# Kernel optimization log

Measured on AMD Instinct MI355X. Metric: run time of the kernel, lower is better.

## Reference

```python
import jax, jax.numpy as jnp
import numpy as np

B, TT, TS, H, O = 16, 512, 512, 1024, 1024


def setup_inputs() -> dict:
    key = jax.random.key(0)
    k1, k2, k3, k4, k5 = jax.random.split(key, 5)
    ht = jax.random.normal(k1, (B, TT, H), dtype=jnp.float32)
    hs = jax.random.normal(k2, (B, TS, H), dtype=jnp.float32)
    source = jax.random.randint(k3, (B, TS), 0, 10000, dtype=jnp.int32)
    # glorot-like scaling for weights
    W_a = jax.random.normal(k4, (H, H), dtype=jnp.float32) * (2.0 / (H + H)) ** 0.5
    W_c = jax.random.normal(k5, (2 * H, O), dtype=jnp.float32) * (2.0 / (2 * H + O)) ** 0.5
    b = jnp.zeros((O,), dtype=jnp.float32)
    return {"ht": ht, "hs": hs, "source": source, "W_a": W_a, "W_c": W_c, "b": b}


def reference(ht, hs, source, W_a, W_c, b):
    # score = ht . (hs @ W_a)^T : [B, Tt, Ts]
    keys = jnp.einsum('bsk,kl->bsl', hs, W_a)
    score = jnp.einsum('btk,bsk->bts', ht, keys)
    # stable exp with max subtraction (matches original manual softmax)
    score = jnp.exp(score - jnp.max(score, axis=-1, keepdims=True))
    # sequence mask from count of non-pad (non-zero) source tokens
    lens = jnp.sum((source != 0).astype(jnp.int32), axis=1)          # [B]
    mask = (jnp.arange(TS)[None, :] < lens[:, None]).astype(score.dtype)  # [B, Ts]
    score = score * mask[:, None, :]
    a = score / jnp.sum(score, axis=-1, keepdims=True)               # [B, Tt, Ts]
    c = jnp.einsum('bts,bsk->btk', a, hs)                            # context [B, Tt, H]
    h = jnp.concatenate([c, ht], axis=-1)                            # [B, Tt, 2H]
    return jnp.tanh(jnp.einsum('btk,kl->btl', h, W_c) + b)
```

## Files before the change

### kernel.cpp

```cpp
#include <hip/hip_runtime.h>
#include <math.h>

typedef unsigned short u16;
typedef unsigned int u32;

using f32x4 = __attribute__((ext_vector_type(4))) float;
using s16x8 = __attribute__((ext_vector_type(8))) short;
using f16x8 = __attribute__((ext_vector_type(8))) _Float16;
using u32x4 = __attribute__((ext_vector_type(4))) u32;

#define DEVI static __device__ __forceinline__

#define BB 16
#define TT 512
#define TS 512
#define HH 1024
#define OO 1024

DEVI void split_bf(float x, u16& hb, u16& lb) {
    u32 xb = __float_as_uint(x);
    float hf = __uint_as_float(xb & 0xffff0000u);
    hb = (u16)(xb >> 16);
    lb = (u16)(__float_as_uint(x - hf) >> 16);
}

DEVI float ub(u16 h) { return __uint_as_float((u32)h << 16); }

template <int PREC> struct FragT;
template <> struct FragT<0> { using T = s16x8; };
template <> struct FragT<1> { using T = f16x8; };

DEVI f32x4 mfma16(s16x8 a, s16x8 b, f32x4 c) {
    return __builtin_amdgcn_mfma_f32_16x16x32_bf16(a, b, c, 0, 0, 0);
}
DEVI f32x4 mfma16(f16x8 a, f16x8 b, f32x4 c) {
    return __builtin_amdgcn_mfma_f32_16x16x32_f16(a, b, c, 0, 0, 0);
}

DEVI void gl16(const void* g, void* l) {
    __builtin_amdgcn_global_load_lds(
        (__attribute__((address_space(1))) const void*)g,
        (__attribute__((address_space(3))) void*)l, 16, 0, 0);
}

__global__ void prep1_kernel(const float* __restrict__ hs,
                             u16* __restrict__ rhi, u16* __restrict__ rlo,
                             u16* __restrict__ thi,
                             const float* __restrict__ Wa,
                             u16* __restrict__ whi, u16* __restrict__ wlo,
                             const int* __restrict__ src, int* __restrict__ lens) {
    __shared__ float tile[32][33];
    __shared__ int part[4];
    int id = blockIdx.x;
    int tid = threadIdx.x;
    int tx = tid & 31, ty = tid >> 5;
    if (id < 8192) {
        int bx = id & 31, by = (id >> 5) & 15, bz = id >> 9;
        long boff = (long)bz * TS * HH;
        const float* s = hs + boff;
        u16* rh = rhi + boff;
        u16* rl = rlo + boff;
        u16* th = thi + boff;
        int c0 = bx * 32, r0 = by * 32;
#pragma unroll
        for (int i = 0; i < 32; i += 8) {
            long o = (long)(r0 + ty + i) * HH + (c0 + tx);
            float v = s[o];
            tile[ty + i][tx] = v;
            u16 hb, lb;
            split_bf(v, hb, lb);
            rh[o] = hb;
            rl[o] = lb;
        }
        __syncthreads();
#pragma unroll
        for (int i = 0; i < 32; i += 8) {
            long o = (long)(c0 + ty + i) * TS + (r0 + tx);
            th[o] = __builtin_bit_cast(u16, (_Float16)tile[tx][ty + i]);
        }
    } else if (id < 8192 + 1024) {
        int id2 = id - 8192;
        int bx = id2 & 31, by = id2 >> 5;
        int c0 = bx * 32, r0 = by * 32;
#pragma unroll
        for (int i = 0; i < 32; i += 8)
            tile[ty + i][tx] = Wa[(long)(r0 + ty + i) * HH + (c0 + tx)];
        __syncthreads();
#pragma unroll
        for (int i = 0; i < 32; i += 8) {
            u16 hb, lb;
            split_bf(tile[tx][ty + i], hb, lb);
            long o = (long)(c0 + ty + i) * HH + (r0 + tx);
            whi[o] = hb;
            wlo[o] = lb;
        }
    } else {
        int b = id - (8192 + 1024);
        int v0 = (src[b * TS + tid] != 0) ? 1 : 0;
        int v1 = (src[b * TS + 256 + tid] != 0) ? 1 : 0;
        unsigned long long m0 = __ballot(v0);
        unsigned long long m1 = __ballot(v1);
        if ((tid & 63) == 0) part[tid >> 6] = __popcll(m0) + __popcll(m1);
        __syncthreads();
        if (tid == 0) lens[b] = part[0] + part[1] + part[2] + part[3];
    }
}

__global__ void prep2_kernel(const float* __restrict__ ht, u16* __restrict__ htF,
                             const float* __restrict__ Wc, u16* __restrict__ wcthi) {
    __shared__ float tile[32][33];
    int id = blockIdx.x;
    int tid = threadIdx.x;
    if (id < 4096) {
        long i = ((long)id * 256 + tid) * 8;
        float4 v0 = *(const float4*)(ht + i);
        float4 v1 = *(const float4*)(ht + i + 4);
        float fv[8] = {v0.x, v0.y, v0.z, v0.w, v1.x, v1.y, v1.z, v1.w};
        f16x8 o;
#pragma unroll
        for (int j = 0; j < 8; ++j) o[j] = (_Float16)fv[j];
        *(f16x8*)(htF + i) = o;
    } else {
        int id2 = id - 4096;
        int bx = id2 & 31, by = id2 >> 5;
        int tx = tid & 31, ty = tid >> 5;
        int c0 = bx * 32, r0 = by * 32;
#pragma unroll
        for (int i = 0; i < 32; i += 8)
            tile[ty + i][tx] = Wc[(long)(r0 + ty + i) * OO + (c0 + tx)];
        __syncthreads();
#pragma unroll
        for (int i = 0; i < 32; i += 8) {
            long o = (long)(c0 + ty + i) * (2 * HH) + (r0 + tx);
            wcthi[o] = __builtin_bit_cast(u16, (_Float16)tile[tx][ty + i]);
        }
    }
}

__global__ void softmax_mask_kernel(u16* __restrict__ h0, u16* __restrict__ l0,
                                    const u16* __restrict__ h1, const u16* __restrict__ l1,
                                    const int* __restrict__ lens) {
    long row = blockIdx.x;
    int len = lens[blockIdx.x >> 9];
    int lane = threadIdx.x;
    long o = row * TS + 8 * lane;
    s16x8 vh0 = *(const s16x8*)(h0 + o);
    s16x8 vl0 = *(const s16x8*)(l0 + o);
    s16x8 vh1 = *(const s16x8*)(h1 + o);
    s16x8 vl1 = *(const s16x8*)(l1 + o);
    float f[8];
#pragma unroll
    for (int i = 0; i < 8; ++i)
        f[i] = (ub((u16)vh0[i]) + ub((u16)vl0[i])) + (ub((u16)vh1[i]) + ub((u16)vl1[i]));
    float m = f[0];
#pragma unroll
    for (int i = 1; i < 8; ++i) m = fmaxf(m, f[i]);
#pragma unroll
    for (int os = 32; os > 0; os >>= 1) m = fmaxf(m, __shfl_xor(m, os));
    float e[8];
    float sum = 0.f;
#pragma unroll
    for (int i = 0; i < 8; ++i) {
        e[i] = (8 * lane + i < len) ? expf(f[i] - m) : 0.f;
        sum += e[i];
    }
#pragma unroll
    for (int os = 32; os > 0; os >>= 1) sum += __shfl_xor(sum, os);
    float inv = 1.0f / sum;
    f16x8 p;
#pragma unroll
    for (int i = 0; i < 8; ++i) p[i] = (_Float16)(e[i] * inv);
    *(f16x8*)(h0 + o) = p;
}

template <int PREC, int TERMS, int EPI, int ACON, int KSPLIT, int SWZ>
__global__ __launch_bounds__(512, 2)
void gemm_p(const u16* __restrict__ Ahi, const u16* __restrict__ Alo,
            const u16* __restrict__ A2,
            const u16* __restrict__ Bhi, const u16* __restrict__ Blo,
            float* __restrict__ C, u16* __restrict__ Chi, u16* __restrict__ Clo,
            const float* __restrict__ bias,
            int N, int K, int lda, int ldb,
            long sA, long sB, long sC, long sKh) {
    constexpr int SUBS = (TERMS == 3) ? 1 : 2;
    constexpr int BKI = 32 * SUBS;
    constexpr int SUBU = (TERMS == 3) ? 24576 : 12288;
    constexpr int BUFU = 24576;
    constexpr int AHo = 0;
    constexpr int ALof = 8192;
    constexpr int BHo = (TERMS == 3) ? 16384 : 8192;
    constexpr int BLof = 20480;

    __shared__ u16 lds[3 * BUFU];

    int bx, by, bz = 0;
    if (SWZ) {
        int id = blockIdx.x;
        int ns = ((id & 7) << 5) | (id >> 3);
        by = ns >> 3;
        bx = ns & 7;
    } else {
        bx = blockIdx.x;
        by = blockIdx.y;
        bz = blockIdx.z;
    }
    int kh = 0;
    if (KSPLIT == 2) {
        kh = bz & 1;
        bz >>= 1;
    }
    if (!ACON) {
        Ahi += (long)bz * sA + (long)kh * K;
        if (TERMS == 3) Alo += (long)bz * sA + (long)kh * K;
    }
    Bhi += (long)bz * sB + (long)kh * K;
    if (TERMS == 3) Blo += (long)bz * sB + (long)kh * K;

    int tid = threadIdx.x;
    int lane = tid & 63;
    int wave = tid >> 6;
    int wm = (wave >> 1) * 64;
    int wn = (wave & 1) * 64;
    int fr = lane & 15;
    int kq = lane >> 4;
    int m0 = by * 256;
    int n0 = bx * 128;

    f32x4 acc[4][4];
#pragma unroll
    for (int i = 0; i < 4; ++i)
#pragma unroll
        for (int j = 0; j < 4; ++j) acc[i][j] = (f32x4){0.f, 0.f, 0.f, 0.f};

    auto stage_arr = [&](int dst, const u16* g, int r0, int ldg, int k0, int cnt) {
#pragma unroll
        for (int h = 0; h < cnt; ++h) {
            int vt = tid + h * 512;
            int row = vt >> 2;
            int ls = (vt & 3) ^ ((row >> 1) & 3);
            const u16* gp = g + (long)(r0 + row) * ldg + (k0 + 8 * ls);
            u16* lp = lds + dst + ((tid & ~63) + h * 512) * 8;
            gl16(gp, lp);
        }
    };
    auto stage = [&](int bi, int t) {
#pragma unroll
        for (int s = 0; s < SUBS; ++s) {
            int ks = t * BKI + s * 32;
            int sb = bi * BUFU + s * ((TERMS == 3) ? 0 : SUBU);
            if (ACON) {
                if (ks < HH)
                    stage_arr(sb + AHo, Ahi, m0, lda, ks, 2);
                else
                    stage_arr(sb + AHo, A2, m0, lda, ks - HH, 2);
            } else {
                stage_arr(sb + AHo, Ahi, m0, lda, ks, 2);
                if (TERMS == 3) stage_arr(sb + ALof, Alo, m0, lda, ks, 2);
            }
            stage_arr(sb + BHo, Bhi, n0, ldb, ks, 1);
            if (TERMS == 3) stage_arr(sb + BLof, Blo, n0, ldb, ks, 1);
        }
    };

    const int NTI = K / BKI;
    stage(0, 0);
    stage(1, 1);
    stage(2, 2);
    asm volatile("s_waitcnt vmcnt(12)" ::: "memory");
    __builtin_amdgcn_sched_barrier(0);
    __builtin_amdgcn_s_barrier();
    __builtin_amdgcn_sched_barrier(0);

    using FT = typename FragT<PREC>::T;
    for (int t = 0; t < NTI; ++t) {
        if (t >= 1 && t + 2 < NTI) stage((t + 2) % 3, t + 2);

        const u16* Lb = lds + (t % 3) * BUFU;
#pragma unroll
        for (int s = 0; s < SUBS; ++s) {
            const u16* Ls = Lb + s * SUBU;
            FT afh[4], afl[4], bfh[4], bfl[4];
#pragma unroll
            for (int i = 0; i < 4; ++i) {
                int ra = wm + i * 16 + fr;
                int rb = wn + i * 16 + fr;
                int oa = ra * 32 + ((kq ^ ((ra >> 1) & 3)) << 3);
                int ob = rb * 32 + ((kq ^ ((rb >> 1) & 3)) << 3);
                afh[i] = *(const FT*)(Ls + AHo + oa);
                bfh[i] = *(const FT*)(Ls + BHo + ob);
                if (TERMS == 3) {
                    afl[i] = *(const FT*)(Ls + ALof + oa);
                    bfl[i] = *(const FT*)(Ls + BLof + ob);
                }
            }
            __builtin_amdgcn_s_setprio(1);
#pragma unroll
            for (int i = 0; i < 4; ++i)
#pragma unroll
                for (int j = 0; j < 4; ++j) {
                    acc[i][j] = mfma16(afh[i], bfh[j], acc[i][j]);
                    if (TERMS == 3) {
                        acc[i][j] = mfma16(afl[i], bfh[j], acc[i][j]);
                        acc[i][j] = mfma16(afh[i], bfl[j], acc[i][j]);
                    }
                }
            __builtin_amdgcn_s_setprio(0);
        }
        if (t < NTI - 1) {
            __builtin_amdgcn_sched_barrier(0);
            if (t + 2 < NTI)
                asm volatile("s_waitcnt vmcnt(6)" ::: "memory");
            else
                asm volatile("s_waitcnt vmcnt(0)" ::: "memory");
            __builtin_amdgcn_sched_barrier(0);
            __builtin_amdgcn_s_barrier();
            __builtin_amdgcn_sched_barrier(0);
        }
    }

    long obase = (long)bz * sC + (long)kh * sKh;
    int fq = (lane >> 4) * 4;
#pragma unroll
    for (int i = 0; i < 4; ++i)
#pragma unroll
        for (int j = 0; j < 4; ++j)
#pragma unroll
            for (int g = 0; g < 4; ++g) {
                int row = m0 + wm + i * 16 + fq + g;
                int col = n0 + wn + j * 16 + fr;
                long idx = obase + (long)row * N + col;
                float v = acc[i][j][g];
                if constexpr (EPI == 1) {
                    u16 h2, l2;
                    split_bf(v, h2, l2);
                    Chi[idx] = h2;
                    Clo[idx] = l2;
                } else if constexpr (EPI == 2) {
                    float x = v + bias[col];
                    float t2 = __expf(2.f * x);
                    C[idx] = 1.f - 2.f * __builtin_amdgcn_rcpf(t2 + 1.f);
                } else {
                    Chi[idx] = __builtin_bit_cast(u16, (_Float16)v);
                }
            }
}

template <int PREC, int ASRC, int EPI, int TERMS, int KSPLIT, bool SWZ>
__global__ __launch_bounds__(256, 2)
void gemm_u(const u16* __restrict__ Ahi, const u16* __restrict__ Alo,
            const float* __restrict__ Af,
            const u16* __restrict__ Bhi, const u16* __restrict__ Blo,
            float* __restrict__ C, u16* __restrict__ Chi, u16* __restrict__ Clo,
            const float* __restrict__ bias,
            int M, int N, int K, int lda, int ldb,
            long sA, long sB, long sC, long sKh) {
    int bx, by, bz;
    if (SWZ) {
        int id = blockIdx.x;
        int ns = ((id & 7) << 6) | (id >> 3);
        bx = ns & 7;
        by = ns >> 3;
        bz = 0;
    } else {
        bx = blockIdx.x;
        by = blockIdx.y;
        bz = blockIdx.z;
    }
    int kh = 0;
    if (KSPLIT == 2) {
        kh = bz & 1;
        bz >>= 1;
    }
    if (ASRC == 0) {
        Ahi += (long)bz * sA + (long)kh * K;
        if (TERMS == 3) Alo += (long)bz * sA + (long)kh * K;
    } else if (ASRC == 1) {
        Af += (long)bz * sA + (long)kh * K;
    }
    Bhi += (long)bz * sB + (long)kh * K;
    if (TERMS == 3) Blo += (long)bz * sB + (long)kh * K;

    int n0 = bx * 128;
    int m0 = by * 128;

    constexpr int NARR = (TERMS == 3) ? 4 : 2;
    constexpr int AH = 0, AL = 1;
    constexpr int BH = (TERMS == 3) ? 2 : 1;
    constexpr int BL = 3;
    __shared__ u16 lds[2][NARR * 4096];

    int tid = threadIdx.x;
    int lane = tid & 63;
    int wave = tid >> 6;
    int wm = (wave >> 1) * 64;
    int wn = (wave & 1) * 64;
    int fr = lane & 15;
    int kq = lane >> 4;

    f32x4 acc[4][4];
#pragma unroll
    for (int i = 0; i < 4; ++i)
#pragma unroll
        for (int j = 0; j < 4; ++j) acc[i][j] = (f32x4){0.f, 0.f, 0.f, 0.f};

    auto stage_gl = [&](int bufi, int arr, const u16* g, int r0, int ldg, int k0) {
#pragma unroll
        for (int h = 0; h < 2; ++h) {
            int vt = tid + h * 256;
            int row = vt >> 2;
            int ls = (vt & 3) ^ ((row >> 1) & 3);
            const u16* gp = g + (long)(r0 + row) * ldg + (k0 + 8 * ls);
            u16* lp = &lds[bufi][arr * 4096 + (vt >> 6) * 512];
            gl16(gp, lp);
        }
    };

    auto stage_a_f32 = [&](int bufi, const float* g, int ldg, int kk) {
        int r = tid >> 1;
        int hf = (tid & 1) * 16;
        const float* p = g + (long)(m0 + r) * ldg + kk + hf;
        float4 a0 = *(const float4*)(p + 0);
        float4 a1 = *(const float4*)(p + 4);
        float4 a2 = *(const float4*)(p + 8);
        float4 a3 = *(const float4*)(p + 12);
        float fv[16] = {a0.x, a0.y, a0.z, a0.w, a1.x, a1.y, a1.z, a1.w,
                        a2.x, a2.y, a2.z, a2.w, a3.x, a3.y, a3.z, a3.w};
        u16 hb[16], lb[16];
#pragma unroll
        for (int i = 0; i < 16; ++i) {
            if constexpr (PREC == 0)
                split_bf(fv[i], hb[i], lb[i]);
            else
                hb[i] = __builtin_bit_cast(u16, (_Float16)fv[i]);
        }
        int sw = (r >> 1) & 3;
        int ls0 = hf >> 3;
        u32x4 h0 = {(u32)hb[0] | ((u32)hb[1] << 16), (u32)hb[2] | ((u32)hb[3] << 16),
                    (u32)hb[4] | ((u32)hb[5] << 16), (u32)hb[6] | ((u32)hb[7] << 16)};
        u32x4 h1 = {(u32)hb[8] | ((u32)hb[9] << 16), (u32)hb[10] | ((u32)hb[11] << 16),
                    (u32)hb[12] | ((u32)hb[13] << 16), (u32)hb[14] | ((u32)hb[15] << 16)};
        u16* ah = &lds[bufi][AH * 4096 + r * 32];
        *(u32x4*)(ah + (((ls0 + 0) ^ sw) << 3)) = h0;
        *(u32x4*)(ah + (((ls0 + 1) ^ sw) << 3)) = h1;
        if constexpr (TERMS == 3) {
            u32x4 l0 = {(u32)lb[0] | ((u32)lb[1] << 16), (u32)lb[2] | ((u32)lb[3] << 16),
                        (u32)lb[4] | ((u32)lb[5] << 16), (u32)lb[6] | ((u32)lb[7] << 16)};
            u32x4 l1 = {(u32)lb[8] | ((u32)lb[9] << 16), (u32)lb[10] | ((u32)lb[11] << 16),
                        (u32)lb[12] | ((u32)lb[13] << 16), (u32)lb[14] | ((u32)lb[15] << 16)};
            u16* al = &lds[bufi][AL * 4096 + r * 32];
            *(u32x4*)(al + (((ls0 + 0) ^ sw) << 3)) = l0;
            *(u32x4*)(al + (((ls0 + 1) ^ sw) << 3)) = l1;
        }
    };

    auto stage = [&](int bufi, int t) {
        int k0 = t * 32;
        stage_gl(bufi, BH, Bhi, n0, ldb, k0);
        if (TERMS == 3) stage_gl(bufi, BL, Blo, n0, ldb, k0);
        if (ASRC == 0) {
            stage_gl(bufi, AH, Ahi, m0, lda, k0);
            if (TERMS == 3) stage_gl(bufi, AL, Alo, m0, lda, k0);
        } else {
            stage_a_f32(bufi, Af, lda, k0);
        }
    };

    const int NT = K / 32;
    stage(0, 0);
    __syncthreads();
    int cur = 0;
    using FT = typename FragT<PREC>::T;
    for (int t = 0; t < NT; ++t) {
        if (t + 1 < NT) stage(cur ^ 1, t + 1);

        const u16* L = lds[cur];
        FT afh[4], afl[4], bfh[4], bfl[4];
#pragma unroll
        for (int i = 0; i < 4; ++i) {
            int ra = wm + i * 16 + fr;
            int rb = wn + i * 16 + fr;
            int oa = ra * 32 + ((kq ^ ((ra >> 1) & 3)) << 3);
            int ob = rb * 32 + ((kq ^ ((rb >> 1) & 3)) << 3);
            afh[i] = *(const FT*)(L + AH * 4096 + oa);
            bfh[i] = *(const FT*)(L + BH * 4096 + ob);
            if (TERMS == 3) {
                afl[i] = *(const FT*)(L + AL * 4096 + oa);
                bfl[i] = *(const FT*)(L + BL * 4096 + ob);
            }
        }
#pragma unroll
        for (int i = 0; i < 4; ++i)
#pragma unroll
            for (int j = 0; j < 4; ++j) {
                acc[i][j] = mfma16(afh[i], bfh[j], acc[i][j]);
                if (TERMS == 3) {
                    acc[i][j] = mfma16(afl[i], bfh[j], acc[i][j]);
                    acc[i][j] = mfma16(afh[i], bfl[j], acc[i][j]);
                }
            }
        __syncthreads();
        cur ^= 1;
    }

    long obase = (long)bz * sC + (long)kh * sKh;
    int fq = (lane >> 4) * 4;
#pragma unroll
    for (int i = 0; i < 4; ++i)
#pragma unroll
        for (int j = 0; j < 4; ++j)
#pragma unroll
            for (int g = 0; g < 4; ++g) {
                int row = m0 + wm + i * 16 + fq + g;
                int col = n0 + wn + j * 16 + fr;
                long idx = obase + (long)row * N + col;
                float v = acc[i][j][g];
                if constexpr (EPI == 1) {
                    u16 h2, l2;
                    split_bf(v, h2, l2);
                    Chi[idx] = h2;
                    Clo[idx] = l2;
                } else if constexpr (EPI == 2) {
                    float x = v + bias[col];
                    float t2 = __expf(2.f * x);
                    C[idx] = 1.f - 2.f * __builtin_amdgcn_rcpf(t2 + 1.f);
                } else {
                    Chi[idx] = __builtin_bit_cast(u16, (_Float16)v);
                }
            }
}

extern "C" void kernel_launch(void* const* d_in, const int* in_sizes, int n_in,
                              void* d_out, int out_size, void* d_ws, size_t ws_size,
                              hipStream_t stream) {
    const float* ht = (const float*)d_in[0];
    const float* hs = (const float*)d_in[1];
    const int* source = (const int*)d_in[2];
    const float* Wa = (const float*)d_in[3];
    const float* Wc = (const float*)d_in[4];
    const float* bias = (const float*)d_in[5];
    float* out = (float*)d_out;

    char* w = (char*)d_ws;
    size_t off = 0;
    auto alloc = [&](size_t bytes) -> void* {
        void* p = w + off;
        off += (bytes + 255) & ~(size_t)255;
        return p;
    };
    int* lens = (int*)alloc(256);
    u16* keysHi = (u16*)alloc((size_t)BB * TS * HH * 2);
    u16* keysLo = (u16*)alloc((size_t)BB * TS * HH * 2);
    u16* hsRHi = (u16*)alloc((size_t)BB * TS * HH * 2);
    u16* hsRLo = (u16*)alloc((size_t)BB * TS * HH * 2);
    u16* hsTHi = (u16*)alloc((size_t)BB * HH * TS * 2);
    u16* WaTHi = (u16*)alloc((size_t)HH * HH * 2);
    u16* WaTLo = (u16*)alloc((size_t)HH * HH * 2);
    u16* scoreH0 = hsRHi;
    u16* scoreH1 = hsRHi + (size_t)BB * TT * TS;
    u16* scoreL0 = hsRLo;
    u16* scoreL1 = hsRLo + (size_t)BB * TT * TS;
    u16* cHi = keysHi;
    u16* WcTHi = scoreL0;
    u16* htF = hsTHi;
    u16* prob = scoreH0;

    prep1_kernel<<<8192 + 1024 + 16, 256, 0, stream>>>(
        hs, hsRHi, hsRLo, hsTHi, Wa, WaTHi, WaTLo, source, lens);

    gemm_p<0, 3, 1, 0, 1, 1><<<256, 512, 0, stream>>>(
        hsRHi, hsRLo, nullptr, WaTHi, WaTLo,
        nullptr, keysHi, keysLo, nullptr,
        HH, HH, HH, HH, 0, 0, 0, 0);

    gemm_u<0, 1, 1, 3, 2, false><<<dim3(TS / 128, TT / 128, 2 * BB), 256, 0, stream>>>(
        nullptr, nullptr, ht, keysHi, keysLo,
        nullptr, scoreH0, scoreL0, nullptr,
        TT, TS, HH / 2, HH, HH,
        (long)TT * HH, (long)TS * HH, (long)TT * TS, (long)BB * TT * TS);

    softmax_mask_kernel<<<BB * TT, 64, 0, stream>>>(scoreH0, scoreL0, scoreH1, scoreL1, lens);

    gemm_u<1, 0, 3, 1, 1, false><<<dim3(HH / 128, TT / 128, BB), 256, 0, stream>>>(
        prob, nullptr, nullptr, hsTHi, nullptr,
        nullptr, cHi, nullptr, nullptr,
        TT, HH, TS, TS, TS,
        (long)TT * TS, (long)HH * TS, (long)TT * HH, 0);

    prep2_kernel<<<4096 + 2048, 256, 0, stream>>>(ht, htF, Wc, WcTHi);

    gemm_p<1, 1, 2, 1, 1, 1><<<256, 512, 0, stream>>>(
        cHi, nullptr, htF, WcTHi, nullptr,
        out, nullptr, nullptr, bias,
        OO, 2 * HH, HH, 2 * HH, 0, 0, 0, 0);
}
```

Baseline: 190.2 us.

## Read B fragments directly from global memory and use double-buffered A staging

The persistent GEMM kernel no longer stages the weight (B) operand through LDS. Each wave loads its B fragments straight from global memory, relying on cache hits since the weight matrix is small and shared across blocks. LDS now holds only the A operand with a deeper K step, and the triple-buffer pipeline becomes a double buffer with full vmcnt(0) waits. This frees LDS space and lowers LDS traffic, but it puts global-load latency directly in front of the MFMAs and removes part of the prefetch overlap.

```diff
diff --git a/kernel.cpp b/kernel.cpp
--- a/kernel.cpp
+++ b/kernel.cpp
@@ -173,48 +173,26 @@
     *(f16x8*)(h0 + o) = p;
 }
 
-template <int PREC, int TERMS, int EPI, int ACON, int KSPLIT, int SWZ>
+template <int PREC, int TERMS, int EPI, int ACON>
 __global__ __launch_bounds__(512, 2)
-void gemm_p(const u16* __restrict__ Ahi, const u16* __restrict__ Alo,
+void gemm_q(const u16* __restrict__ Ahi, const u16* __restrict__ Alo,
             const u16* __restrict__ A2,
             const u16* __restrict__ Bhi, const u16* __restrict__ Blo,
             float* __restrict__ C, u16* __restrict__ Chi, u16* __restrict__ Clo,
             const float* __restrict__ bias,
-            int N, int K, int lda, int ldb,
-            long sA, long sB, long sC, long sKh) {
-    constexpr int SUBS = (TERMS == 3) ? 1 : 2;
+            int N, int K, int lda, int ldb) {
+    constexpr int SUBS = (TERMS == 3) ? 2 : 4;
     constexpr int BKI = 32 * SUBS;
-    constexpr int SUBU = (TERMS == 3) ? 24576 : 12288;
-    constexpr int BUFU = 24576;
-    constexpr int AHo = 0;
-    constexpr int ALof = 8192;
-    constexpr int BHo = (TERMS == 3) ? 16384 : 8192;
-    constexpr int BLof = 20480;
-
-    __shared__ u16 lds[3 * BUFU];
-
-    int bx, by, bz = 0;
-    if (SWZ) {
-        int id = blockIdx.x;
-        int ns = ((id & 7) << 5) | (id >> 3);
-        by = ns >> 3;
-        bx = ns & 7;
-    } else {
-        bx = blockIdx.x;
-        by = blockIdx.y;
-        bz = blockIdx.z;
-    }
-    int kh = 0;
-    if (KSPLIT == 2) {
-        kh = bz & 1;
-        bz >>= 1;
-    }
-    if (!ACON) {
-        Ahi += (long)bz * sA + (long)kh * K;
-        if (TERMS == 3) Alo += (long)bz * sA + (long)kh * K;
-    }
-    Bhi += (long)bz * sB + (long)kh * K;
-    if (TERMS == 3) Blo += (long)bz * sB + (long)kh * K;
+    constexpr int ASZ = 8192;
+    constexpr int NARR = (TERMS == 3) ? 2 : 1;
+    constexpr int BUFU = SUBS * NARR * ASZ;
+
+    __shared__ u16 lds[2 * BUFU];
+
+    int id = blockIdx.x;
+    int ns = ((id & 7) << 5) | (id >> 3);
+    int by = ns >> 3;
+    int bx = ns & 7;
 
     int tid = threadIdx.x;
     int lane = tid & 63;
@@ -232,13 +210,13 @@
 #pragma unroll
         for (int j = 0; j < 4; ++j) acc[i][j] = (f32x4){0.f, 0.f, 0.f, 0.f};
 
-    auto stage_arr = [&](int dst, const u16* g, int r0, int ldg, int k0, int cnt) {
-#pragma unroll
-        for (int h = 0; h < cnt; ++h) {
+    auto stage_arr = [&](int dst, const u16* g, int k0) {
+#pragma unroll
+        for (int h = 0; h < 2; ++h) {
             int vt = tid + h * 512;
             int row = vt >> 2;
             int ls = (vt & 3) ^ ((row >> 1) & 3);
-            const u16* gp = g + (long)(r0 + row) * ldg + (k0 + 8 * ls);
+            const u16* gp = g + (long)(m0 + row) * lda + (k0 + 8 * ls);
             u16* lp = lds + dst + ((tid & ~63) + h * 512) * 8;
             gl16(gp, lp);
         }
@@ -247,51 +225,48 @@
 #pragma unroll
         for (int s = 0; s < SUBS; ++s) {
             int ks = t * BKI + s * 32;
-            int sb = bi * BUFU + s * ((TERMS == 3) ? 0 : SUBU);
+            int sb = bi * BUFU + s * NARR * ASZ;
             if (ACON) {
                 if (ks < HH)
-                    stage_arr(sb + AHo, Ahi, m0, lda, ks, 2);
+                    stage_arr(sb, Ahi, ks);
                 else
-                    stage_arr(sb + AHo, A2, m0, lda, ks - HH, 2);
+                    stage_arr(sb, A2, ks - HH);
             } else {
-                stage_arr(sb + AHo, Ahi, m0, lda, ks, 2);
-                if (TERMS == 3) stage_arr(sb + ALof, Alo, m0, lda, ks, 2);
-            }
-            stage_arr(sb + BHo, Bhi, n0, ldb, ks, 1);
-            if (TERMS == 3) stage_arr(sb + BLof, Blo, n0, ldb, ks, 1);
+                stage_arr(sb, Ahi, ks);
+                if (TERMS == 3) stage_arr(sb + ASZ, Alo, ks);
+            }
         }
     };
 
     const int NTI = K / BKI;
     stage(0, 0);
-    stage(1, 1);
-    stage(2, 2);
-    asm volatile("s_waitcnt vmcnt(12)" ::: "memory");
+    asm volatile("s_waitcnt vmcnt(0)" ::: "memory");
     __builtin_amdgcn_sched_barrier(0);
     __builtin_amdgcn_s_barrier();
     __builtin_amdgcn_sched_barrier(0);
 
     using FT = typename FragT<PREC>::T;
     for (int t = 0; t < NTI; ++t) {
-        if (t >= 1 && t + 2 < NTI) stage((t + 2) % 3, t + 2);
-
-        const u16* Lb = lds + (t % 3) * BUFU;
+        if (t + 1 < NTI) stage((t + 1) & 1, t + 1);
+
+        const u16* Lb = lds + (t & 1) * BUFU;
 #pragma unroll
         for (int s = 0; s < SUBS; ++s) {
-            const u16* Ls = Lb + s * SUBU;
+            const u16* Ls = Lb + s * NARR * ASZ;
+            int ks = t * BKI + s * 32;
             FT afh[4], afl[4], bfh[4], bfl[4];
 #pragma unroll
             for (int i = 0; i < 4; ++i) {
                 int ra = wm + i * 16 + fr;
-                int rb = wn + i * 16 + fr;
                 int oa = ra * 32 + ((kq ^ ((ra >> 1) & 3)) << 3);
-                int ob = rb * 32 + ((kq ^ ((rb >> 1) & 3)) << 3);
-                afh[i] = *(const FT*)(Ls + AHo + oa);
-                bfh[i] = *(const FT*)(Ls + BHo + ob);
-                if (TERMS == 3) {
-                    afl[i] = *(const FT*)(Ls + ALof + oa);
-                    bfl[i] = *(const FT*)(Ls + BLof + ob);
-                }
+                afh[i] = *(const FT*)(Ls + oa);
+                if (TERMS == 3) afl[i] = *(const FT*)(Ls + ASZ + oa);
+            }
+#pragma unroll
+            for (int j = 0; j < 4; ++j) {
+                long rb = n0 + wn + j * 16 + fr;
+                bfh[j] = *(const FT*)(Bhi + rb * ldb + ks + kq * 8);
+                if (TERMS == 3) bfl[j] = *(const FT*)(Blo + rb * ldb + ks + kq * 8);
             }
             __builtin_amdgcn_s_setprio(1);
 #pragma unroll
@@ -308,17 +283,13 @@
         }
         if (t < NTI - 1) {
             __builtin_amdgcn_sched_barrier(0);
-            if (t + 2 < NTI)
-                asm volatile("s_waitcnt vmcnt(6)" ::: "memory");
-            else
-                asm volatile("s_waitcnt vmcnt(0)" ::: "memory");
+            asm volatile("s_waitcnt vmcnt(0)" ::: "memory");
             __builtin_amdgcn_sched_barrier(0);
             __builtin_amdgcn_s_barrier();
             __builtin_amdgcn_sched_barrier(0);
         }
     }
 
-    long obase = (long)bz * sC + (long)kh * sKh;
     int fq = (lane >> 4) * 4;
 #pragma unroll
     for (int i = 0; i < 4; ++i)
@@ -328,7 +299,7 @@
             for (int g = 0; g < 4; ++g) {
                 int row = m0 + wm + i * 16 + fq + g;
                 int col = n0 + wn + j * 16 + fr;
-                long idx = obase + (long)row * N + col;
+                long idx = (long)row * N + col;
                 float v = acc[i][j][g];
                 if constexpr (EPI == 1) {
                     u16 h2, l2;
@@ -567,10 +538,10 @@
     prep1_kernel<<<8192 + 1024 + 16, 256, 0, stream>>>(
         hs, hsRHi, hsRLo, hsTHi, Wa, WaTHi, WaTLo, source, lens);
 
-    gemm_p<0, 3, 1, 0, 1, 1><<<256, 512, 0, stream>>>(
+    gemm_q<0, 3, 1, 0><<<256, 512, 0, stream>>>(
         hsRHi, hsRLo, nullptr, WaTHi, WaTLo,
         nullptr, keysHi, keysLo, nullptr,
-        HH, HH, HH, HH, 0, 0, 0, 0);
+        HH, HH, HH, HH);
 
     gemm_u<0, 1, 1, 3, 2, false><<<dim3(TS / 128, TT / 128, 2 * BB), 256, 0, stream>>>(
         nullptr, nullptr, ht, keysHi, keysLo,
@@ -588,8 +559,8 @@
 
     prep2_kernel<<<4096 + 2048, 256, 0, stream>>>(ht, htF, Wc, WcTHi);
 
-    gemm_p<1, 1, 2, 1, 1, 1><<<256, 512, 0, stream>>>(
+    gemm_q<1, 1, 2, 1><<<256, 512, 0, stream>>>(
         cHi, nullptr, htF, WcTHi, nullptr,
         out, nullptr, nullptr, bias,
-        OO, 2 * HH, HH, 2 * HH, 0, 0, 0, 0);
-}
+        OO, 2 * HH, HH, 2 * HH);
+}
```

New measurement: 267.1 us. 40.4% more time.
